# Kernel optimization log

Hardware: AMD Instinct MI355X
Metric: run time of the kernel (lower is better)

Reference implementation:

```python
import jax, jax.numpy as jnp
import numpy as np
from jax import lax

B, L, H, K = 256, 512, 768, 64


def setup_inputs() -> dict:
    key = jax.random.key(0)
    k1, k2, k3, k4, k5 = jax.random.split(key, 5)
    features = jax.random.normal(k1, (B, L, H), dtype=jnp.float32)
    W = jax.random.normal(k2, (H, K), dtype=jnp.float32) * 0.02
    b = jnp.zeros((K,), dtype=jnp.float32)
    transition = jax.random.normal(k3, (K, K), dtype=jnp.float32)
    tags = jax.random.randint(k4, (B, L), 0, K, dtype=jnp.int64)
    # variable sentence lengths in decreasing order (repo sorts batches by length)
    lengths = jnp.sort(jax.random.randint(k5, (B,), L // 4, L + 1))[::-1]
    mask = jnp.arange(L)[None, :] < lengths[:, None]  # (B, L) bool, pads at end
    return {"features": features, "W": W, "b": b, "transition": transition,
            "tags": tags, "mask": mask}


def reference(features, W, b, transition, tags, mask):
    # encode: hidden2tag linear (dropout is identity in eval)
    emit = jnp.einsum("blh,hk->blk", features, W) + b  # (B, L, K)
    maskf = mask.astype(emit.dtype)

    # gold path score
    gold_emit = jnp.take_along_axis(emit, tags[:, :, None], axis=2)[..., 0]  # (B, L)
    trans_sc = transition[tags[:, :-1], tags[:, 1:]]                          # (B, L-1)
    score = gold_emit.at[:, 1:].add(trans_sc)
    total_score = (score * maskf).sum(axis=1)                                 # (B,)

    # CRF forward algorithm (log partition) via scan over time
    d0 = emit[:, 0]  # (B, K)
    emit_t = jnp.moveaxis(emit[:, 1:], 1, 0)  # (L-1, B, K)
    mask_t = mask[:, 1:].T                    # (L-1, B)

    def step(d, xs):
        e_t, m_t = xs
        # log_sum[b, j, k] = d[b, j] + transition[j, k] + e_t[b, k]
        log_sum = d[:, :, None] + transition[None, :, :] + e_t[:, None, :]
        d_new = jax.scipy.special.logsumexp(log_sum, axis=1)  # (B, K)
        d = jnp.where(m_t[:, None], d_new, d)  # finished sequences keep old d
        return d, None

    d, _ = lax.scan(step, d0, (emit_t, mask_t))
    log_z = jax.scipy.special.logsumexp(d, axis=1)  # (B,)

    return log_z - total_score  # negative log-likelihood per sentence, (B,)
```

## Files before the change

### kernel.cpp

```cpp
#include <hip/hip_runtime.h>
#include <hip/hip_bf16.h>
#include <string.h>

#define B_ 256
#define L_ 512
#define H_ 768
#define K_ 64
#define WT_OFF 33554432

typedef float  float4v  __attribute__((ext_vector_type(4)));
typedef float  float2v  __attribute__((ext_vector_type(2)));
typedef short  short8v  __attribute__((ext_vector_type(8)));

union BFragU { uint4 u4; short8v s8; };

__device__ inline unsigned short f2bf_bits(float f) {
    union { float f; unsigned int u; } c; c.f = f;
    unsigned int u = c.u;
    u += 0x7fffu + ((u >> 16) & 1u);
    return (unsigned short)(u >> 16);
}

__device__ inline float2v mk2(float x, float y) { float2v v; v.x = x; v.y = y; return v; }

__global__ void wt_transpose(const float* __restrict__ W, unsigned int* __restrict__ Wt) {
    int k = blockIdx.x;
    int j = threadIdx.x;
    float a = W[(size_t)(2 * j) * K_ + k];
    float b = W[(size_t)(2 * j + 1) * K_ + k];
    unsigned int u = (unsigned int)f2bf_bits(a) | ((unsigned int)f2bf_bits(b) << 16);
    Wt[k * (H_ / 2) + j] = u;
}

struct StageS {
    uint4  b[4];
    float4 a[2];
};

__device__ __forceinline__ void load_stageS(StageS& s, const float* __restrict__ A,
        const unsigned short* __restrict__ Wt, int rowbase, int ks, int lm, int lq) {
    #pragma unroll
    for (int nt = 0; nt < 4; ++nt)
        s.b[nt] = *reinterpret_cast<const uint4*>(
            Wt + (size_t)(lm + nt * 16) * H_ + ks * 32 + lq * 8);
    const float* ap = A + (size_t)rowbase * H_ + ks * 32 + lq * 8;
    s.a[0] = *reinterpret_cast<const float4*>(ap);
    s.a[1] = *reinterpret_cast<const float4*>(ap + 4);
}

__device__ __forceinline__ void consume_stageS(const StageS& s, float4v acc[4]) {
    short8v bfrag[4];
    #pragma unroll
    for (int nt = 0; nt < 4; ++nt) { BFragU u; u.u4 = s.b[nt]; bfrag[nt] = u.s8; }
    __hip_bfloat162 tt[4];
    tt[0] = __float22bfloat162_rn(make_float2(s.a[0].x, s.a[0].y));
    tt[1] = __float22bfloat162_rn(make_float2(s.a[0].z, s.a[0].w));
    tt[2] = __float22bfloat162_rn(make_float2(s.a[1].x, s.a[1].y));
    tt[3] = __float22bfloat162_rn(make_float2(s.a[1].z, s.a[1].w));
    short8v afrag;
    memcpy(&afrag, tt, 16);
    #pragma unroll
    for (int nt = 0; nt < 4; ++nt)
        acc[nt] = __builtin_amdgcn_mfma_f32_16x16x32_bf16(afrag, bfrag[nt], acc[nt], 0, 0, 0);
}

__global__ __launch_bounds__(256, 3)
void emit_gemm(const float* __restrict__ A, const unsigned short* __restrict__ Wt,
               const float* __restrict__ bias, const int* __restrict__ mask,
               float* __restrict__ emit) {
    const int tid  = threadIdx.x;
    const int lane = tid & 63;
    const int wid  = tid >> 6;
    const int lm   = lane & 15;
    const int lq   = lane >> 4;
    const int r0   = blockIdx.x * 64;
    if (mask[r0 + wid * 16] == 0) return;
    const int rowbase = r0 + wid * 16 + lm;

    float4v acc[4];
    #pragma unroll
    for (int nt = 0; nt < 4; ++nt) acc[nt] = (float4v)0.f;

    StageS s0, s1;
    load_stageS(s0, A, Wt, rowbase, 0, lm, lq);
    #pragma unroll 1
    for (int ks = 0; ks < 24; ks += 2) {
        load_stageS(s1, A, Wt, rowbase, ks + 1, lm, lq);
        consume_stageS(s0, acc);
        load_stageS(s0, A, Wt, rowbase, (ks + 2 < 24) ? ks + 2 : 23, lm, lq);
        consume_stageS(s1, acc);
    }

    float bv[4];
    #pragma unroll
    for (int nt = 0; nt < 4; ++nt) bv[nt] = bias[nt * 16 + lm];
    const int rowb = r0 + wid * 16 + lq * 4;
    #pragma unroll
    for (int nt = 0; nt < 4; ++nt) {
        int col = nt * 16 + lm;
        #pragma unroll
        for (int r = 0; r < 4; ++r)
            emit[(size_t)(rowb + r) * K_ + col] = acc[nt][r] + bv[nt];
    }
}

__global__ __launch_bounds__(64, 1)
void crf_scan(const float* __restrict__ emit, const float* __restrict__ T,
              const int* __restrict__ tags, const int* __restrict__ mask,
              float* __restrict__ out) {
    const int b    = blockIdx.x;
    const int lane = threadIdx.x;
    __shared__ __align__(16) float qbuf[2][64];

    int len = 0;
    #pragma unroll
    for (int j = 0; j < 8; ++j) len += (mask[b * L_ + j * 64 + lane] != 0);
    #pragma unroll
    for (int off = 32; off; off >>= 1) len += __shfl_xor(len, off, 64);

    float2v et2[32];
    #pragma unroll
    for (int j = 0; j < 32; ++j) {
        et2[j].x = __expf(T[(2 * j) * K_ + lane]);
        et2[j].y = __expf(T[(2 * j + 1) * K_ + lane]);
    }

    const float* eb = emit + (size_t)b * L_ * K_;

    float sc = 0.f;
    for (int tt = lane; tt < len; tt += 64) {
        int tg = tags[b * L_ + tt];
        sc += eb[(size_t)tt * K_ + tg];
        if (tt > 0) sc += T[tags[b * L_ + tt - 1] * K_ + tg];
    }
    #pragma unroll
    for (int off = 32; off; off >>= 1) sc += __shfl_xor(sc, off, 64);

    float e00 = eb[lane];
    float M = __int_as_float(__builtin_amdgcn_readfirstlane(__float_as_int(e00)));
    float q = __expf(e00 - M);
    qbuf[0][lane] = q;

    float eA[4], eB[4];
    #pragma unroll
    for (int i = 0; i < 4; ++i) {
        eA[i] = eb[(size_t)(1 + i) * K_ + lane];
        eB[i] = eb[(size_t)(5 + i) * K_ + lane];
    }

    int eps = 0;
    int t = 1;

    auto step = [&](float& ereg) {
        float e = ereg;
        int tp = t + 8; if (tp > L_ - 1) tp = L_ - 1;
        ereg = eb[(size_t)tp * K_ + lane];
        float ef = __int_as_float(__builtin_amdgcn_readfirstlane(__float_as_int(e)));
        float delta = (float)eps * 0.69314718f + ef;
        M += delta;
        float f = __expf(e - delta);

        const float4* qb4 = reinterpret_cast<const float4*>(&qbuf[(t + 1) & 1][0]);
        float2v a0 = mk2(0.f, 0.f), a1 = mk2(0.f, 0.f);
        float2v a2 = mk2(0.f, 0.f), a3 = mk2(0.f, 0.f);
        #pragma unroll
        for (int r = 0; r < 16; r += 2) {
            float4 p0 = qb4[r];
            float4 p1 = qb4[r + 1];
            a0 += mk2(p0.x, p0.y) * et2[2 * r];
            a1 += mk2(p0.z, p0.w) * et2[2 * r + 1];
            a2 += mk2(p1.x, p1.y) * et2[2 * r + 2];
            a3 += mk2(p1.z, p1.w) * et2[2 * r + 3];
        }
        float2v s2 = (a0 + a1) + (a2 + a3);
        float s = s2.x + s2.y;
        unsigned su = (unsigned)__builtin_amdgcn_readfirstlane(__float_as_int(s));
        eps = (int)((su >> 23) & 0xffu) - 127;
        q = s * f;
        qbuf[t & 1][lane] = q;
        ++t;
    };

    #pragma unroll 1
    while (t < len) {
        step(eA[0]); if (t >= len) break;
        step(eA[1]); if (t >= len) break;
        step(eA[2]); if (t >= len) break;
        step(eA[3]); if (t >= len) break;
        step(eB[0]); if (t >= len) break;
        step(eB[1]); if (t >= len) break;
        step(eB[2]); if (t >= len) break;
        step(eB[3]);
    }

    float z = q;
    #pragma unroll
    for (int off = 32; off; off >>= 1) z += __shfl_xor(z, off, 64);
    if (lane == 0) out[b] = M + __logf(z) - sc;
}

extern "C" void kernel_launch(void* const* d_in, const int* in_sizes, int n_in,
                              void* d_out, int out_size, void* d_ws, size_t ws_size,
                              hipStream_t stream) {
    const float* feat = (const float*)d_in[0];
    const float* W    = (const float*)d_in[1];
    const float* bias = (const float*)d_in[2];
    const float* T    = (const float*)d_in[3];
    const int*   tags = (const int*)d_in[4];
    const int*   mask = (const int*)d_in[5];
    float* out  = (float*)d_out;
    float* emit = (float*)d_ws;
    unsigned int*   WtW = (unsigned int*)((char*)d_ws + WT_OFF);
    unsigned short* Wt  = (unsigned short*)WtW;

    hipLaunchKernelGGL(wt_transpose, dim3(K_),   dim3(H_ / 2), 0, stream, W, WtW);
    hipLaunchKernelGGL(emit_gemm,    dim3(2048), dim3(256),    0, stream, feat, Wt, bias, mask, emit);
    hipLaunchKernelGGL(crf_scan,     dim3(B_),   dim3(64),     0, stream, emit, T, tags, mask, out);
}
```

Baseline: 705.7 us.

## Split CRF gold-score onto second wave, widen accumulators, nontemporal feature loads

The CRF scan kernel now launches two waves per sentence. The second wave computes the gold-path score in parallel while the first runs the sequential forward recursion, and the two combine through shared memory after a barrier. The per-step matrix-vector loop uses eight independent accumulators instead of four to shorten dependency chains. In the GEMM, feature loads are marked nontemporal to avoid polluting the cache with streamed data. The cost is an extra barrier and a doubled block size for the scan kernel.

New measurement: 719.3 us. About the same (+1.9%).

```diff
diff --git a/kernel.cpp b/kernel.cpp
--- a/kernel.cpp
+++ b/kernel.cpp
@@ -33,8 +33,8 @@
 }
 
 struct StageS {
-    uint4  b[4];
-    float4 a[2];
+    uint4   b[4];
+    float4v a[2];
 };
 
 __device__ __forceinline__ void load_stageS(StageS& s, const float* __restrict__ A,
@@ -44,8 +44,8 @@
         s.b[nt] = *reinterpret_cast<const uint4*>(
             Wt + (size_t)(lm + nt * 16) * H_ + ks * 32 + lq * 8);
     const float* ap = A + (size_t)rowbase * H_ + ks * 32 + lq * 8;
-    s.a[0] = *reinterpret_cast<const float4*>(ap);
-    s.a[1] = *reinterpret_cast<const float4*>(ap + 4);
+    s.a[0] = __builtin_nontemporal_load(reinterpret_cast<const float4v*>(ap));
+    s.a[1] = __builtin_nontemporal_load(reinterpret_cast<const float4v*>(ap + 4));
 }
 
 __device__ __forceinline__ void consume_stageS(const StageS& s, float4v acc[4]) {
@@ -104,13 +104,15 @@
     }
 }
 
-__global__ __launch_bounds__(64, 1)
+__global__ __launch_bounds__(128, 1)
 void crf_scan(const float* __restrict__ emit, const float* __restrict__ T,
               const int* __restrict__ tags, const int* __restrict__ mask,
               float* __restrict__ out) {
     const int b    = blockIdx.x;
-    const int lane = threadIdx.x;
+    const int lane = threadIdx.x & 63;
+    const int wid  = threadIdx.x >> 6;
     __shared__ __align__(16) float qbuf[2][64];
+    __shared__ float scsh;
 
     int len = 0;
     #pragma unroll
@@ -118,85 +120,98 @@
     #pragma unroll
     for (int off = 32; off; off >>= 1) len += __shfl_xor(len, off, 64);
 
-    float2v et2[32];
-    #pragma unroll
-    for (int j = 0; j < 32; ++j) {
-        et2[j].x = __expf(T[(2 * j) * K_ + lane]);
-        et2[j].y = __expf(T[(2 * j + 1) * K_ + lane]);
+    const float* eb = emit + (size_t)b * L_ * K_;
+
+    float M = 0.f, z = 0.f;
+
+    if (wid == 1) {
+        float sc = 0.f;
+        for (int tt = lane; tt < len; tt += 64) {
+            int tg = tags[b * L_ + tt];
+            sc += eb[(size_t)tt * K_ + tg];
+            if (tt > 0) sc += T[tags[b * L_ + tt - 1] * K_ + tg];
+        }
+        #pragma unroll
+        for (int off = 32; off; off >>= 1) sc += __shfl_xor(sc, off, 64);
+        if (lane == 0) scsh = sc;
+    } else {
+        float2v et2[32];
+        #pragma unroll
+        for (int j = 0; j < 32; ++j) {
+            et2[j].x = __expf(T[(2 * j) * K_ + lane]);
+            et2[j].y = __expf(T[(2 * j + 1) * K_ + lane]);
+        }
+
+        float e00 = eb[lane];
+        M = __int_as_float(__builtin_amdgcn_readfirstlane(__float_as_int(e00)));
+        float q = __expf(e00 - M);
+        qbuf[0][lane] = q;
+
+        float eA[4], eB[4];
+        #pragma unroll
+        for (int i = 0; i < 4; ++i) {
+            eA[i] = eb[(size_t)(1 + i) * K_ + lane];
+            eB[i] = eb[(size_t)(5 + i) * K_ + lane];
+        }
+
+        int eps = 0;
+        int t = 1;
+
+        auto step = [&](float& ereg) {
+            float e = ereg;
+            int tp = t + 8; if (tp > L_ - 1) tp = L_ - 1;
+            ereg = eb[(size_t)tp * K_ + lane];
+            float ef = __int_as_float(__builtin_amdgcn_readfirstlane(__float_as_int(e)));
+            float delta = (float)eps * 0.69314718f + ef;
+            M += delta;
+            float f = __expf(e - delta);
+
+            const float4* qb4 = reinterpret_cast<const float4*>(&qbuf[(t + 1) & 1][0]);
+            float2v c0 = mk2(0.f, 0.f), c1 = mk2(0.f, 0.f), c2 = mk2(0.f, 0.f), c3 = mk2(0.f, 0.f);
+            float2v c4 = mk2(0.f, 0.f), c5 = mk2(0.f, 0.f), c6 = mk2(0.f, 0.f), c7 = mk2(0.f, 0.f);
+            #pragma unroll
+            for (int r = 0; r < 16; r += 4) {
+                float4 p0 = qb4[r];
+                float4 p1 = qb4[r + 1];
+                float4 p2 = qb4[r + 2];
+                float4 p3 = qb4[r + 3];
+                c0 += mk2(p0.x, p0.y) * et2[2 * r];
+                c1 += mk2(p0.z, p0.w) * et2[2 * r + 1];
+                c2 += mk2(p1.x, p1.y) * et2[2 * r + 2];
+                c3 += mk2(p1.z, p1.w) * et2[2 * r + 3];
+                c4 += mk2(p2.x, p2.y) * et2[2 * r + 4];
+                c5 += mk2(p2.z, p2.w) * et2[2 * r + 5];
+                c6 += mk2(p3.x, p3.y) * et2[2 * r + 6];
+                c7 += mk2(p3.z, p3.w) * et2[2 * r + 7];
+            }
+            float2v s2 = ((c0 + c1) + (c2 + c3)) + ((c4 + c5) + (c6 + c7));
+            float s = s2.x + s2.y;
+            unsigned su = (unsigned)__builtin_amdgcn_readfirstlane(__float_as_int(s));
+            eps = (int)((su >> 23) & 0xffu) - 127;
+            q = s * f;
+            qbuf[t & 1][lane] = q;
+            ++t;
+        };
+
+        #pragma unroll 1
+        while (t < len) {
+            step(eA[0]); if (t >= len) break;
+            step(eA[1]); if (t >= len) break;
+            step(eA[2]); if (t >= len) break;
+            step(eA[3]); if (t >= len) break;
+            step(eB[0]); if (t >= len) break;
+            step(eB[1]); if (t >= len) break;
+            step(eB[2]); if (t >= len) break;
+            step(eB[3]);
+        }
+
+        z = q;
+        #pragma unroll
+        for (int off = 32; off; off >>= 1) z += __shfl_xor(z, off, 64);
     }
 
-    const float* eb = emit + (size_t)b * L_ * K_;
-
-    float sc = 0.f;
-    for (int tt = lane; tt < len; tt += 64) {
-        int tg = tags[b * L_ + tt];
-        sc += eb[(size_t)tt * K_ + tg];
-        if (tt > 0) sc += T[tags[b * L_ + tt - 1] * K_ + tg];
-    }
-    #pragma unroll
-    for (int off = 32; off; off >>= 1) sc += __shfl_xor(sc, off, 64);
-
-    float e00 = eb[lane];
-    float M = __int_as_float(__builtin_amdgcn_readfirstlane(__float_as_int(e00)));
-    float q = __expf(e00 - M);
-    qbuf[0][lane] = q;
-
-    float eA[4], eB[4];
-    #pragma unroll
-    for (int i = 0; i < 4; ++i) {
-        eA[i] = eb[(size_t)(1 + i) * K_ + lane];
-        eB[i] = eb[(size_t)(5 + i) * K_ + lane];
-    }
-
-    int eps = 0;
-    int t = 1;
-
-    auto step = [&](float& ereg) {
-        float e = ereg;
-        int tp = t + 8; if (tp > L_ - 1) tp = L_ - 1;
-        ereg = eb[(size_t)tp * K_ + lane];
-        float ef = __int_as_float(__builtin_amdgcn_readfirstlane(__float_as_int(e)));
-        float delta = (float)eps * 0.69314718f + ef;
-        M += delta;
-        float f = __expf(e - delta);
-
-        const float4* qb4 = reinterpret_cast<const float4*>(&qbuf[(t + 1) & 1][0]);
-        float2v a0 = mk2(0.f, 0.f), a1 = mk2(0.f, 0.f);
-        float2v a2 = mk2(0.f, 0.f), a3 = mk2(0.f, 0.f);
-        #pragma unroll
-        for (int r = 0; r < 16; r += 2) {
-            float4 p0 = qb4[r];
-            float4 p1 = qb4[r + 1];
-            a0 += mk2(p0.x, p0.y) * et2[2 * r];
-            a1 += mk2(p0.z, p0.w) * et2[2 * r + 1];
-            a2 += mk2(p1.x, p1.y) * et2[2 * r + 2];
-            a3 += mk2(p1.z, p1.w) * et2[2 * r + 3];
-        }
-        float2v s2 = (a0 + a1) + (a2 + a3);
-        float s = s2.x + s2.y;
-        unsigned su = (unsigned)__builtin_amdgcn_readfirstlane(__float_as_int(s));
-        eps = (int)((su >> 23) & 0xffu) - 127;
-        q = s * f;
-        qbuf[t & 1][lane] = q;
-        ++t;
-    };
-
-    #pragma unroll 1
-    while (t < len) {
-        step(eA[0]); if (t >= len) break;
-        step(eA[1]); if (t >= len) break;
-        step(eA[2]); if (t >= len) break;
-        step(eA[3]); if (t >= len) break;
-        step(eB[0]); if (t >= len) break;
-        step(eB[1]); if (t >= len) break;
-        step(eB[2]); if (t >= len) break;
-        step(eB[3]);
-    }
-
-    float z = q;
-    #pragma unroll
-    for (int off = 32; off; off >>= 1) z += __shfl_xor(z, off, 64);
-    if (lane == 0) out[b] = M + __logf(z) - sc;
+    __syncthreads();
+    if (wid == 0 && lane == 0) out[b] = M + __logf(z) - scsh;
 }
 
 extern "C" void kernel_launch(void* const* d_in, const int* in_sizes, int n_in,
@@ -215,5 +230,5 @@
 
     hipLaunchKernelGGL(wt_transpose, dim3(K_),   dim3(H_ / 2), 0, stream, W, WtW);
     hipLaunchKernelGGL(emit_gemm,    dim3(2048), dim3(256),    0, stream, feat, Wt, bias, mask, emit);
-    hipLaunchKernelGGL(crf_scan,     dim3(B_),   dim3(64),     0, stream, emit, T, tags, mask, out);
-}
+    hipLaunchKernelGGL(crf_scan,     dim3(B_),   dim3(128),    0, stream, emit, T, tags, mask, out);
+}
```
